# Kernel tuning notes

Measured on AMD Instinct MI355X. Metric: run time of the kernel, lower is better.

## Reference

```python
import jax, jax.numpy as jnp
import numpy as np

BS, C_REP, H, W = 24, 16, 320, 320
NUM_CLASSES = 4
NUM_MICRO_PROTO = 4
MOMENTUM = 0.99


def setup_inputs() -> dict:
    key = jax.random.key(0)
    k1, k2, k3, k4, k5, k6 = jax.random.split(key, 6)
    rep = jax.random.normal(k1, (BS, C_REP, H, W), dtype=jnp.float32)
    proto_match_idx = jax.random.randint(k2, (BS, H, W, NUM_CLASSES), 0, NUM_MICRO_PROTO, dtype=jnp.int32)
    target = jax.random.randint(k3, (BS, H, W), 0, NUM_CLASSES, dtype=jnp.int32)
    select_mask = jax.random.randint(k4, (H, W), 0, 2, dtype=jnp.int32)
    cond = jax.random.randint(k5, (BS, H, W), 0, 2, dtype=jnp.int32).astype(jnp.bool_)
    protos = jax.random.normal(k6, (NUM_CLASSES, NUM_MICRO_PROTO, C_REP), dtype=jnp.float32)
    return {"rep": rep, "proto_match_idx": proto_match_idx, "target": target,
            "select_mask": select_mask, "cond": cond, "protos": protos}


def reference(rep, proto_match_idx, target, select_mask, cond, protos):
    # Vectorized equivalent of NNet_2d.update_proto:
    #   select pixels where select_mask==1, target!=0, cond True;
    #   group them by (class, micro_proto_idx) where micro_proto_idx is the
    #   column of proto_match_idx chosen by the target class;
    #   take the mean rep per group and EMA-update that prototype.
    bs, c, Hh, Ww = rep.shape
    Ccls, M, _ = protos.shape
    n_seg = Ccls * M

    rep_flat = rep.transpose(0, 2, 3, 1).reshape(-1, c)            # [N, c]
    tgt = target.reshape(-1)                                        # [N]
    pmi = proto_match_idx.reshape(-1, Ccls)                         # [N, Ccls]
    # micro-proto index matched at the target class for each pixel
    pidx = jnp.take_along_axis(pmi, tgt[:, None], axis=-1)[:, 0]    # [N]

    valid = (select_mask[None, :, :] == 1) & (target != 0) & cond   # [bs,H,W]
    w = valid.reshape(-1).astype(rep_flat.dtype)                    # [N]

    seg = tgt * M + pidx                                            # [N] in [0, n_seg)
    sums = jax.ops.segment_sum(rep_flat * w[:, None], seg, num_segments=n_seg)  # [n_seg, c]
    counts = jax.ops.segment_sum(w, seg, num_segments=n_seg)        # [n_seg]

    mean = sums / jnp.maximum(counts, 1.0)[:, None]                 # segment means
    protos_flat = protos.reshape(n_seg, c)
    has_members = (counts > 0)[:, None]
    new_protos = jnp.where(has_members,
                           MOMENTUM * protos_flat + (1.0 - MOMENTUM) * mean,
                           protos_flat)
    return new_protos.reshape(Ccls, M, c)
```

## Files before the change

kernel.cpp:

```cpp
#include <hip/hip_runtime.h>

#define BS 24
#define CREP 16
#define HH 320
#define WW 320
#define HW (HH * WW)
#define TOTAL (BS * HW)
#define NMP 4
#define NSEG 16
#define NELEM 272
#define MOM 0.99f

__global__ void detect_cond_kernel(const unsigned int* __restrict__ cond_u32,
                                   int* __restrict__ flag) {
    bool big = false;
    for (int i = threadIdx.x; i < 256; i += 64)
        big |= (cond_u32[i] > 1u);
    unsigned long long b = __ballot(big);
    if (threadIdx.x == 0) flag[0] = (b != 0ull) ? 1 : 0;
}

__global__ __launch_bounds__(256) void accum_kernel(
    const float* __restrict__ rep,
    const int* __restrict__ pmi,
    const int* __restrict__ tgt,
    const int* __restrict__ smask,
    const unsigned char* __restrict__ cond_b,
    const int* __restrict__ flag,
    float* __restrict__ partials,
    int NB)
{
    __shared__ float lds[288];
    for (int i = threadIdx.x; i < 288; i += 256) lds[i] = 0.0f;
    __syncthreads();

    const int byte_layout = flag[0];
    const int* cond_i = (const int*)cond_b;

    const int stride = gridDim.x * 256;
    for (int n = blockIdx.x * 256 + threadIdx.x; n < TOTAL; n += stride) {
        const int t  = tgt[n];
        const int hw = n % HW;
        bool v = (t != 0) && (smask[hw] == 1);
        if (v) {
            const int cv = byte_layout ? (int)cond_b[n] : cond_i[n];
            v = (cv != 0);
        }
        if (v) {
            const int b    = n / HW;
            const int pidx = pmi[n * 4 + t];
            const int seg  = t * NMP + pidx;
            const float* r = rep + (size_t)b * CREP * HW + hw;
            atomicAdd(&lds[272 + seg], 1.0f);
#pragma unroll
            for (int c = 0; c < CREP; ++c)
                atomicAdd(&lds[seg * 17 + c], r[c * HW]);
        }
    }
    __syncthreads();

    for (int e = threadIdx.x; e < NELEM; e += 256) {
        float val = (e < 256) ? lds[(e >> 4) * 17 + (e & 15)]
                              : lds[272 + (e - 256)];
        partials[(size_t)e * NB + blockIdx.x] = val;
    }
}

__global__ __launch_bounds__(256) void reduce_kernel(
    const float* __restrict__ partials,
    const float* __restrict__ protos,
    float* __restrict__ out,
    int NB)
{
    const int w    = (blockIdx.x * 256 + threadIdx.x) >> 6;
    const int lane = threadIdx.x & 63;
    const int seg  = w >> 4;

    float s = 0.0f, cnt = 0.0f;
    for (int b = lane; b < NB; b += 64) {
        s   += partials[(size_t)w * NB + b];
        cnt += partials[(size_t)(256 + seg) * NB + b];
    }
#pragma unroll
    for (int off = 32; off > 0; off >>= 1) {
        s   += __shfl_xor(s, off, 64);
        cnt += __shfl_xor(cnt, off, 64);
    }
    if (lane == 0) {
        const float mean = s / fmaxf(cnt, 1.0f);
        out[w] = (cnt > 0.0f) ? (MOM * protos[w] + (1.0f - MOM) * mean)
                              : protos[w];
    }
}

extern "C" void kernel_launch(void* const* d_in, const int* in_sizes, int n_in,
                              void* d_out, int out_size, void* d_ws, size_t ws_size,
                              hipStream_t stream) {
    const float*         rep    = (const float*)d_in[0];
    const int*           pmi    = (const int*)d_in[1];
    const int*           tgt    = (const int*)d_in[2];
    const int*           smask  = (const int*)d_in[3];
    const unsigned char* cond   = (const unsigned char*)d_in[4];
    const float*         protos = (const float*)d_in[5];
    float*               out    = (float*)d_out;

    int NB = (int)((ws_size / sizeof(float) - 16) / NELEM);
    if (NB > 2048) NB = 2048;
    if (NB < 1)    NB = 1;
    float* partials = (float*)d_ws;
    int*   flag     = (int*)d_ws + (size_t)NELEM * NB;

    detect_cond_kernel<<<1, 64, 0, stream>>>((const unsigned int*)cond, flag);
    accum_kernel<<<NB, 256, 0, stream>>>(rep, pmi, tgt, smask, cond, flag,
                                         partials, NB);
    reduce_kernel<<<64, 256, 0, stream>>>(partials, protos, out, NB);
}
```

Measured before the change: 289.9 us.

## Tile accumulation per batch image with vectorized loads and precomputed segment ids

```diff
diff --git a/kernel.cpp b/kernel.cpp
--- a/kernel.cpp
+++ b/kernel.cpp
@@ -10,6 +10,11 @@
 #define NSEG 16
 #define NELEM 272
 #define MOM 0.99f
+
+#define TILE 2048
+#define TPB (TILE / 4 / 256)
+#define NTILES (HW / TILE)
+#define NBLK (BS * NTILES)
 
 __global__ void detect_cond_kernel(const unsigned int* __restrict__ cond_u32,
                                    int* __restrict__ flag) {
@@ -27,69 +32,122 @@
     const int* __restrict__ smask,
     const unsigned char* __restrict__ cond_b,
     const int* __restrict__ flag,
-    float* __restrict__ partials,
-    int NB)
+    float* __restrict__ partials)
 {
-    __shared__ float lds[288];
-    for (int i = threadIdx.x; i < 288; i += 256) lds[i] = 0.0f;
+    __shared__ unsigned int segp[TILE / 4];
+    __shared__ float acc[NSEG * 17];
+    __shared__ float cnt[NSEG];
+
+    for (int i = threadIdx.x; i < NSEG * 17; i += 256) acc[i] = 0.0f;
+    if (threadIdx.x < NSEG) cnt[threadIdx.x] = 0.0f;
     __syncthreads();
 
+    const int b    = blockIdx.x / NTILES;
+    const int tile = blockIdx.x % NTILES;
+    const int hw0  = tile * TILE;
+    const int p0   = b * HW + hw0;
     const int byte_layout = flag[0];
-    const int* cond_i = (const int*)cond_b;
 
-    const int stride = gridDim.x * 256;
-    for (int n = blockIdx.x * 256 + threadIdx.x; n < TOTAL; n += stride) {
-        const int t  = tgt[n];
-        const int hw = n % HW;
-        bool v = (t != 0) && (smask[hw] == 1);
-        if (v) {
-            const int cv = byte_layout ? (int)cond_b[n] : cond_i[n];
-            v = (cv != 0);
+    const int4* tgt4  = (const int4*)(tgt + p0);
+    const int4* sm4   = (const int4*)(smask + hw0);
+    const int4* cond4 = (const int4*)((const int*)cond_b + p0);
+    const unsigned int* condb4 = (const unsigned int*)(cond_b + p0);
+
+#pragma unroll
+    for (int j = 0; j < TPB; ++j) {
+        const int g  = threadIdx.x + j * 256;
+        const int4 t4 = tgt4[g];
+        const int4 s4 = sm4[g];
+        int cc[4];
+        if (byte_layout) {
+            const unsigned int cb = condb4[g];
+            cc[0] = cb & 0xff; cc[1] = (cb >> 8) & 0xff;
+            cc[2] = (cb >> 16) & 0xff; cc[3] = (cb >> 24) & 0xff;
+        } else {
+            const int4 ci = cond4[g];
+            cc[0] = ci.x; cc[1] = ci.y; cc[2] = ci.z; cc[3] = ci.w;
         }
-        if (v) {
-            const int b    = n / HW;
-            const int pidx = pmi[n * 4 + t];
-            const int seg  = t * NMP + pidx;
-            const float* r = rep + (size_t)b * CREP * HW + hw;
-            atomicAdd(&lds[272 + seg], 1.0f);
+        const int tt[4] = {t4.x, t4.y, t4.z, t4.w};
+        const int ss[4] = {s4.x, s4.y, s4.z, s4.w};
+        unsigned int packed = 0;
 #pragma unroll
-            for (int c = 0; c < CREP; ++c)
-                atomicAdd(&lds[seg * 17 + c], r[c * HW]);
+        for (int k = 0; k < 4; ++k) {
+            int seg = 255;
+            if (tt[k] != 0 && ss[k] == 1 && cc[k] != 0) {
+                const int pidx = pmi[(p0 + g * 4 + k) * 4 + tt[k]];
+                seg = tt[k] * NMP + pidx;
+                atomicAdd(&cnt[seg], 1.0f);
+            }
+            packed |= (unsigned int)(seg & 0xff) << (8 * k);
         }
+        segp[g] = packed;
+    }
+    __syncthreads();
+
+    int base[TPB][4];
+#pragma unroll
+    for (int j = 0; j < TPB; ++j) {
+        const unsigned int sp = segp[threadIdx.x + j * 256];
+#pragma unroll
+        for (int k = 0; k < 4; ++k) {
+            const int seg = (sp >> (8 * k)) & 0xff;
+            base[j][k] = (seg == 255) ? -1 : seg * 17;
+        }
+    }
+
+    const float4* r4 = (const float4*)(rep + (size_t)b * CREP * HW + hw0);
+#pragma unroll 1
+    for (int c = 0; c < CREP; c += 2) {
+        float4 va[2][TPB];
+#pragma unroll
+        for (int cc2 = 0; cc2 < 2; ++cc2)
+#pragma unroll
+            for (int j = 0; j < TPB; ++j)
+                va[cc2][j] = r4[(size_t)(c + cc2) * (HW / 4) + threadIdx.x + j * 256];
+#pragma unroll
+        for (int cc2 = 0; cc2 < 2; ++cc2)
+#pragma unroll
+            for (int j = 0; j < TPB; ++j) {
+                const float vv[4] = {va[cc2][j].x, va[cc2][j].y,
+                                     va[cc2][j].z, va[cc2][j].w};
+#pragma unroll
+                for (int k = 0; k < 4; ++k)
+                    if (base[j][k] >= 0)
+                        atomicAdd(&acc[base[j][k] + c + cc2], vv[k]);
+            }
     }
     __syncthreads();
 
     for (int e = threadIdx.x; e < NELEM; e += 256) {
-        float val = (e < 256) ? lds[(e >> 4) * 17 + (e & 15)]
-                              : lds[272 + (e - 256)];
-        partials[(size_t)e * NB + blockIdx.x] = val;
+        const float val = (e < 256) ? acc[(e >> 4) * 17 + (e & 15)]
+                                    : cnt[e - 256];
+        partials[(size_t)e * NBLK + blockIdx.x] = val;
     }
 }
 
 __global__ __launch_bounds__(256) void reduce_kernel(
     const float* __restrict__ partials,
     const float* __restrict__ protos,
-    float* __restrict__ out,
-    int NB)
+    float* __restrict__ out)
 {
     const int w    = (blockIdx.x * 256 + threadIdx.x) >> 6;
     const int lane = threadIdx.x & 63;
     const int seg  = w >> 4;
 
-    float s = 0.0f, cnt = 0.0f;
-    for (int b = lane; b < NB; b += 64) {
-        s   += partials[(size_t)w * NB + b];
-        cnt += partials[(size_t)(256 + seg) * NB + b];
+    float s = 0.0f, cntv = 0.0f;
+    for (int b = lane; b < NBLK; b += 64) {
+        s    += partials[(size_t)w * NBLK + b];
+        cntv += partials[(size_t)(256 + seg) * NBLK + b];
     }
 #pragma unroll
     for (int off = 32; off > 0; off >>= 1) {
-        s   += __shfl_xor(s, off, 64);
-        cnt += __shfl_xor(cnt, off, 64);
+        s    += __shfl_xor(s, off, 64);
+        cntv += __shfl_xor(cntv, off, 64);
     }
     if (lane == 0) {
-        const float mean = s / fmaxf(cnt, 1.0f);
-        out[w] = (cnt > 0.0f) ? (MOM * protos[w] + (1.0f - MOM) * mean)
-                              : protos[w];
+        const float mean = s / fmaxf(cntv, 1.0f);
+        out[w] = (cntv > 0.0f) ? (MOM * protos[w] + (1.0f - MOM) * mean)
+                               : protos[w];
     }
 }
 
@@ -104,14 +162,11 @@
     const float*         protos = (const float*)d_in[5];
     float*               out    = (float*)d_out;
 
-    int NB = (int)((ws_size / sizeof(float) - 16) / NELEM);
-    if (NB > 2048) NB = 2048;
-    if (NB < 1)    NB = 1;
     float* partials = (float*)d_ws;
-    int*   flag     = (int*)d_ws + (size_t)NELEM * NB;
+    int*   flag     = (int*)d_ws + (size_t)NELEM * NBLK;
 
     detect_cond_kernel<<<1, 64, 0, stream>>>((const unsigned int*)cond, flag);
-    accum_kernel<<<NB, 256, 0, stream>>>(rep, pmi, tgt, smask, cond, flag,
-                                         partials, NB);
-    reduce_kernel<<<64, 256, 0, stream>>>(partials, protos, out, NB);
+    accum_kernel<<<NBLK, 256, 0, stream>>>(rep, pmi, tgt, smask, cond, flag,
+                                           partials);
+    reduce_kernel<<<64, 256, 0, stream>>>(partials, protos, out);
 }
```

Result: faster. 282.4 us (-2.6%).

## Split into segment-map pass and MFMA one-hot matmul accumulation

Applied to the files above, without the earlier changes.

```diff
diff --git a/kernel.cpp b/kernel.cpp
--- a/kernel.cpp
+++ b/kernel.cpp
@@ -8,8 +8,16 @@
 #define TOTAL (BS * HW)
 #define NMP 4
 #define NSEG 16
-#define NELEM 272
 #define MOM 0.99f
+
+#define K1_BLOCKS 600
+#define TILE 2048
+#define NTILES (HW / TILE)
+#define NBLK (BS * NTILES)
+
+typedef __attribute__((ext_vector_type(8))) short   bf16x8;
+typedef __attribute__((ext_vector_type(4))) float   f32x4;
+typedef __attribute__((ext_vector_type(4))) unsigned int u32x4;
 
 __global__ void detect_cond_kernel(const unsigned int* __restrict__ cond_u32,
                                    int* __restrict__ flag) {
@@ -20,76 +28,140 @@
     if (threadIdx.x == 0) flag[0] = (b != 0ull) ? 1 : 0;
 }
 
-__global__ __launch_bounds__(256) void accum_kernel(
-    const float* __restrict__ rep,
+__global__ __launch_bounds__(256) void segmap_kernel(
     const int* __restrict__ pmi,
     const int* __restrict__ tgt,
     const int* __restrict__ smask,
     const unsigned char* __restrict__ cond_b,
     const int* __restrict__ flag,
-    float* __restrict__ partials,
-    int NB)
+    unsigned int* __restrict__ segmap32,
+    unsigned int* __restrict__ cnt_part)
 {
-    __shared__ float lds[288];
-    for (int i = threadIdx.x; i < 288; i += 256) lds[i] = 0.0f;
+    __shared__ unsigned int hist[NSEG];
+    if (threadIdx.x < NSEG) hist[threadIdx.x] = 0u;
     __syncthreads();
 
     const int byte_layout = flag[0];
-    const int* cond_i = (const int*)cond_b;
+    const int4* tgt4  = (const int4*)tgt;
+    const int4* cond4 = (const int4*)cond_b;
+    const unsigned int* condb = (const unsigned int*)cond_b;
 
-    const int stride = gridDim.x * 256;
-    for (int n = blockIdx.x * 256 + threadIdx.x; n < TOTAL; n += stride) {
-        const int t  = tgt[n];
-        const int hw = n % HW;
-        bool v = (t != 0) && (smask[hw] == 1);
-        if (v) {
-            const int cv = byte_layout ? (int)cond_b[n] : cond_i[n];
-            v = (cv != 0);
+#pragma unroll
+    for (int i = 0; i < 4; ++i) {
+        const int g = blockIdx.x * 256 + threadIdx.x + i * (K1_BLOCKS * 256);
+        const int p = g * 4;
+        const int hw = p % HW;
+        const int4 t4 = tgt4[g];
+        const int4 s4 = *(const int4*)(smask + hw);
+        int cc[4];
+        if (byte_layout) {
+            const unsigned int cb = condb[g];
+            cc[0] = cb & 0xff; cc[1] = (cb >> 8) & 0xff;
+            cc[2] = (cb >> 16) & 0xff; cc[3] = cb >> 24;
+        } else {
+            const int4 ci = cond4[g];
+            cc[0] = ci.x; cc[1] = ci.y; cc[2] = ci.z; cc[3] = ci.w;
         }
-        if (v) {
-            const int b    = n / HW;
-            const int pidx = pmi[n * 4 + t];
-            const int seg  = t * NMP + pidx;
-            const float* r = rep + (size_t)b * CREP * HW + hw;
-            atomicAdd(&lds[272 + seg], 1.0f);
+        const int tt[4] = {t4.x, t4.y, t4.z, t4.w};
+        const int ss[4] = {s4.x, s4.y, s4.z, s4.w};
+        unsigned int packed = 0;
 #pragma unroll
-            for (int c = 0; c < CREP; ++c)
-                atomicAdd(&lds[seg * 17 + c], r[c * HW]);
+        for (int k = 0; k < 4; ++k) {
+            int seg = 255;
+            if (tt[k] != 0 && ss[k] == 1 && cc[k] != 0) {
+                seg = tt[k] * NMP + pmi[(size_t)(p + k) * 4 + tt[k]];
+                atomicAdd(&hist[seg], 1u);
+            }
+            packed |= (unsigned int)(seg & 0xff) << (8 * k);
         }
+        segmap32[g] = packed;
     }
     __syncthreads();
+    if (threadIdx.x < NSEG)
+        cnt_part[(size_t)threadIdx.x * K1_BLOCKS + blockIdx.x] = hist[threadIdx.x];
+}
 
-    for (int e = threadIdx.x; e < NELEM; e += 256) {
-        float val = (e < 256) ? lds[(e >> 4) * 17 + (e & 15)]
-                              : lds[272 + (e - 256)];
-        partials[(size_t)e * NB + blockIdx.x] = val;
+__global__ __launch_bounds__(256) void accum_kernel(
+    const float* __restrict__ rep,
+    const unsigned char* __restrict__ segmap,
+    float* __restrict__ sum_part)
+{
+    const int b   = blockIdx.x / NTILES;
+    const int hw0 = (blockIdx.x % NTILES) * TILE;
+    const int tid = threadIdx.x;
+    const int l   = tid & 63, wv = tid >> 6;
+    const int ch  = l & 15, grp = l >> 4;
+
+    const float* rbase = rep + ((size_t)b * CREP + ch) * HW + hw0 + grp * 8;
+    const unsigned char* sbase = segmap + (size_t)b * HW + hw0 + grp * 8;
+    const unsigned int chm = (unsigned int)ch;
+    const unsigned int one = 0x3F80u;
+
+    f32x4 acc = {0.f, 0.f, 0.f, 0.f};
+
+#pragma unroll 2
+    for (int it = wv * 32; it < TILE; it += 128) {
+        const float4 v0 = *(const float4*)(rbase + it);
+        const float4 v1 = *(const float4*)(rbase + it + 4);
+        const unsigned int slo = *(const unsigned int*)(sbase + it);
+        const unsigned int shi = *(const unsigned int*)(sbase + it + 4);
+
+        u32x4 au, bu;
+        au[0] = (((slo      ) & 0xff) == chm ? one : 0u) |
+                (((slo >>  8) & 0xff) == chm ? one << 16 : 0u);
+        au[1] = (((slo >> 16) & 0xff) == chm ? one : 0u) |
+                (((slo >> 24) & 0xff) == chm ? one << 16 : 0u);
+        au[2] = (((shi      ) & 0xff) == chm ? one : 0u) |
+                (((shi >>  8) & 0xff) == chm ? one << 16 : 0u);
+        au[3] = (((shi >> 16) & 0xff) == chm ? one : 0u) |
+                (((shi >> 24) & 0xff) == chm ? one << 16 : 0u);
+
+        bu[0] = (__float_as_uint(v0.x) >> 16) | (__float_as_uint(v0.y) & 0xffff0000u);
+        bu[1] = (__float_as_uint(v0.z) >> 16) | (__float_as_uint(v0.w) & 0xffff0000u);
+        bu[2] = (__float_as_uint(v1.x) >> 16) | (__float_as_uint(v1.y) & 0xffff0000u);
+        bu[3] = (__float_as_uint(v1.z) >> 16) | (__float_as_uint(v1.w) & 0xffff0000u);
+
+        acc = __builtin_amdgcn_mfma_f32_16x16x32_bf16(
+            __builtin_bit_cast(bf16x8, au),
+            __builtin_bit_cast(bf16x8, bu), acc, 0, 0, 0);
+    }
+
+    __shared__ float lacc[4][256];
+#pragma unroll
+    for (int r = 0; r < 4; ++r)
+        lacc[wv][(grp * 4 + r) * 16 + ch] = acc[r];
+    __syncthreads();
+    if (tid < 256) {
+        const float s = lacc[0][tid] + lacc[1][tid] + lacc[2][tid] + lacc[3][tid];
+        sum_part[(size_t)tid * NBLK + blockIdx.x] = s;
     }
 }
 
 __global__ __launch_bounds__(256) void reduce_kernel(
-    const float* __restrict__ partials,
+    const float* __restrict__ sum_part,
+    const unsigned int* __restrict__ cnt_part,
     const float* __restrict__ protos,
-    float* __restrict__ out,
-    int NB)
+    float* __restrict__ out)
 {
     const int w    = (blockIdx.x * 256 + threadIdx.x) >> 6;
     const int lane = threadIdx.x & 63;
     const int seg  = w >> 4;
 
-    float s = 0.0f, cnt = 0.0f;
-    for (int b = lane; b < NB; b += 64) {
-        s   += partials[(size_t)w * NB + b];
-        cnt += partials[(size_t)(256 + seg) * NB + b];
-    }
+    float s = 0.f;
+    for (int bb = lane; bb < NBLK; bb += 64)
+        s += sum_part[(size_t)w * NBLK + bb];
+    int cn = 0;
+    for (int bb = lane; bb < K1_BLOCKS; bb += 64)
+        cn += (int)cnt_part[(size_t)seg * K1_BLOCKS + bb];
 #pragma unroll
     for (int off = 32; off > 0; off >>= 1) {
-        s   += __shfl_xor(s, off, 64);
-        cnt += __shfl_xor(cnt, off, 64);
+        s  += __shfl_xor(s, off, 64);
+        cn += __shfl_xor(cn, off, 64);
     }
     if (lane == 0) {
+        const float cnt  = (float)cn;
         const float mean = s / fmaxf(cnt, 1.0f);
-        out[w] = (cnt > 0.0f) ? (MOM * protos[w] + (1.0f - MOM) * mean)
-                              : protos[w];
+        out[w] = (cn > 0) ? (MOM * protos[w] + (1.0f - MOM) * mean) : protos[w];
     }
 }
 
@@ -104,14 +176,16 @@
     const float*         protos = (const float*)d_in[5];
     float*               out    = (float*)d_out;
 
-    int NB = (int)((ws_size / sizeof(float) - 16) / NELEM);
-    if (NB > 2048) NB = 2048;
-    if (NB < 1)    NB = 1;
-    float* partials = (float*)d_ws;
-    int*   flag     = (int*)d_ws + (size_t)NELEM * NB;
+    unsigned char* ws      = (unsigned char*)d_ws;
+    unsigned int* segmap32 = (unsigned int*)ws;
+    float*        sum_part = (float*)(ws + (size_t)TOTAL);
+    unsigned int* cnt_part = (unsigned int*)(ws + (size_t)TOTAL + 256 * NBLK * 4);
+    int*          flag     = (int*)(ws + (size_t)TOTAL + 256 * NBLK * 4 + NSEG * K1_BLOCKS * 4);
 
     detect_cond_kernel<<<1, 64, 0, stream>>>((const unsigned int*)cond, flag);
-    accum_kernel<<<NB, 256, 0, stream>>>(rep, pmi, tgt, smask, cond, flag,
-                                         partials, NB);
-    reduce_kernel<<<64, 256, 0, stream>>>(partials, protos, out, NB);
+    segmap_kernel<<<K1_BLOCKS, 256, 0, stream>>>(pmi, tgt, smask, cond, flag,
+                                                 segmap32, cnt_part);
+    accum_kernel<<<NBLK, 256, 0, stream>>>(rep, (const unsigned char*)segmap32,
+                                           sum_part);
+    reduce_kernel<<<64, 256, 0, stream>>>(sum_part, cnt_part, protos, out);
 }
```

After: 287.3 us. Within noise of the previous version (-0.9%).
